# Kernel optimization log

Hardware: AMD Instinct MI355X
Metric: run time of the kernel (lower is better)

## Reference

```python
import jax, jax.numpy as jnp
import numpy as np

B, N, DIM, HEADS = 4, 1024, 1024, 16
DH = DIM // HEADS
SCALE = 1.0 / np.sqrt(DH)
EPS = 1e-6


def clinear(x, Wr, Wi, br, bi):
    # (a+bi)(Wr+Wi i): real = a Wr^T - b Wi^T, imag = a Wi^T + b Wr^T
    xr, xi = x.real, x.imag
    real = xr @ Wr.T - xi @ Wi.T + br
    imag = xr @ Wi.T + xi @ Wr.T + bi
    return jax.lax.complex(real, imag)


def cln(x, gamma, beta):
    # normalize magnitude over last dim, keep phase
    mag = jnp.abs(x)
    phase = jnp.angle(x)
    mean = jnp.mean(mag, axis=-1, keepdims=True)
    var = jnp.var(mag, axis=-1, keepdims=True)
    nm = (mag - mean) / jnp.sqrt(var + EPS)
    nm = nm * gamma + beta
    return jax.lax.complex(nm * jnp.cos(phase), nm * jnp.sin(phase))


def forward(xr, xi, Wq_r, Wq_i, bq_r, bq_i, Wk_r, Wk_i, bk_r, bk_i,
            Wv_r, Wv_i, bv_r, bv_i, Wo_r, Wo_i, bo_r, bo_i,
            gq, beq, gk, bek, gv, bev):
    x = jax.lax.complex(xr, xi)  # [B,N,D] complex64

    def heads(t):
        return t.reshape(B, N, HEADS, DH).transpose(0, 2, 1, 3)  # [B,H,N,dh]

    Q = heads(cln(clinear(x, Wq_r, Wq_i, bq_r, bq_i), gq, beq))
    K = heads(cln(clinear(x, Wk_r, Wk_i, bk_r, bk_i), gk, bek))
    V = heads(cln(clinear(x, Wv_r, Wv_i, bv_r, bv_i), gv, bev))

    Qf = jnp.fft.fft(Q, axis=2, norm='ortho')
    Kf = jnp.fft.fft(K, axis=2, norm='ortho')
    Vf = jnp.fft.fft(V, axis=2, norm='ortho')

    scores = jnp.einsum('bhnd,bhmd->bhnm', Qf, jnp.conj(Kf)) * SCALE
    attn = jax.nn.softmax(scores.real, axis=-1)  # real-valued softmax
    # attn is real; multiply into complex Vf componentwise
    out_f = jax.lax.complex(jnp.einsum('bhnm,bhmd->bhnd', attn, Vf.real),
                            jnp.einsum('bhnm,bhmd->bhnd', attn, Vf.imag))
    out = jnp.fft.ifft(out_f, axis=2, norm='ortho')
    out = out.transpose(0, 2, 1, 3).reshape(B, N, DIM)
    y = clinear(out, Wo_r, Wo_i, bo_r, bo_i)
    # return real||imag concatenated on last axis (float32 view of complex output)
    return jnp.concatenate([y.real, y.imag], axis=-1)


def setup_inputs() -> dict:
    key = jax.random.key(0)
    ks = jax.random.split(key, 16)
    wscale = np.sqrt(2.0 / (DIM + DIM)).astype(np.float32)
    d = {}
    d['xr'] = jax.random.normal(ks[0], (B, N, DIM), jnp.float32)
    d['xi'] = jax.random.normal(ks[1], (B, N, DIM), jnp.float32)
    i = 2
    for name in ('q', 'k', 'v', 'o'):
        d[f'W{name}_r'] = jax.random.normal(ks[i], (DIM, DIM), jnp.float32) * wscale; i += 1
        d[f'W{name}_i'] = jax.random.normal(ks[i], (DIM, DIM), jnp.float32) * wscale; i += 1
        d[f'b{name}_r'] = jnp.zeros((DIM,), jnp.float32)
        d[f'b{name}_i'] = jnp.zeros((DIM,), jnp.float32)
    for name in ('q', 'k', 'v'):
        d[f'g{name}'] = jnp.ones((DIM,), jnp.float32)
        d[f'be{name}'] = jnp.zeros((DIM,), jnp.float32)
    return d


def reference(xr, xi, Wq_r, Wq_i, bq_r, bq_i, Wk_r, Wk_i, bk_r, bk_i,
              Wv_r, Wv_i, bv_r, bv_i, Wo_r, Wo_i, bo_r, bo_i,
              gq, beq, gk, bek, gv, bev):
    return forward(xr, xi, Wq_r, Wq_i, bq_r, bq_i, Wk_r, Wk_i, bk_r, bk_i,
                   Wv_r, Wv_i, bv_r, bv_i, Wo_r, Wo_i, bo_r, bo_i,
                   gq, beq, gk, bek, gv, bev)
```

## Files before the change

kernel.cpp:

```cpp
#include <hip/hip_runtime.h>
#include <math.h>

#define BB 4
#define NN 1024
#define DIMM 1024
#define HHH 16
#define DHH 64
#define BN 4096
#define EPS_LN 1e-6f

typedef __bf16 bf16_t;
typedef __bf16 bf16x8 __attribute__((ext_vector_type(8)));
typedef __bf16 bf16x4 __attribute__((ext_vector_type(4)));
typedef float f32x4 __attribute__((ext_vector_type(4)));
typedef float f32x16 __attribute__((ext_vector_type(16)));
#define MFMA16(a, b, c) __builtin_amdgcn_mfma_f32_16x16x32_bf16(a, b, c, 0, 0, 0)
#define MFMA32(a, b, c) __builtin_amdgcn_mfma_f32_32x32x16_bf16(a, b, c, 0, 0, 0)
#define AS1 __attribute__((address_space(1)))
#define AS3 __attribute__((address_space(3)))

__device__ inline unsigned pk2(float a, float b) {
  union { bf16_t h[2]; unsigned u; } c;
  c.h[0] = (bf16_t)a; c.h[1] = (bf16_t)b;
  return c.u;
}
union U16 { uint4 u; bf16x8 v; };

__global__ __launch_bounds__(256) void pack_x(
    const float* __restrict__ xr, const float* __restrict__ xi,
    bf16_t* __restrict__ out)
{
  int t = blockIdx.x * 256 + threadIdx.x;
  size_t e = (size_t)t * 8;
  int row = (int)(e >> 11), col = (int)(e & 2047);
  const float* src = (col < 1024) ? (xr + (size_t)row * 1024 + col)
                                  : (xi + (size_t)row * 1024 + col - 1024);
  float4 a = *(const float4*)src;
  float4 b = *(const float4*)(src + 4);
  bf16x8 o;
  o[0] = (bf16_t)a.x; o[1] = (bf16_t)a.y; o[2] = (bf16_t)a.z; o[3] = (bf16_t)a.w;
  o[4] = (bf16_t)b.x; o[5] = (bf16_t)b.y; o[6] = (bf16_t)b.z; o[7] = (bf16_t)b.w;
  *(bf16x8*)(out + e) = o;
}

__global__ __launch_bounds__(256) void pack_w(
    const float* __restrict__ Wr, const float* __restrict__ Wi,
    const float* __restrict__ br, const float* __restrict__ bi,
    bf16_t* __restrict__ Wcat, float* __restrict__ bcat)
{
  int t = blockIdx.x * 256 + threadIdx.x;
  size_t e = (size_t)t * 8;
  int row = (int)(e >> 11), col = (int)(e & 2047);
  const float* src;
  float sgn = 1.f;
  if (row < 1024) {
    if (col < 1024) src = Wr + (size_t)row * 1024 + col;
    else          { src = Wi + (size_t)row * 1024 + col - 1024; sgn = -1.f; }
  } else {
    int r2 = row - 1024;
    if (col < 1024) src = Wi + (size_t)r2 * 1024 + col;
    else            src = Wr + (size_t)r2 * 1024 + col - 1024;
  }
  float4 a = *(const float4*)src;
  float4 b = *(const float4*)(src + 4);
  bf16x8 o;
  o[0] = (bf16_t)(sgn * a.x); o[1] = (bf16_t)(sgn * a.y);
  o[2] = (bf16_t)(sgn * a.z); o[3] = (bf16_t)(sgn * a.w);
  o[4] = (bf16_t)(sgn * b.x); o[5] = (bf16_t)(sgn * b.y);
  o[6] = (bf16_t)(sgn * b.z); o[7] = (bf16_t)(sgn * b.w);
  *(bf16x8*)(Wcat + e) = o;
  if (e < 2048) {
#pragma unroll
    for (int j = 0; j < 8; ++j) {
      int n = (int)e + j;
      bcat[n] = (n < 1024) ? br[n] : bi[n - 1024];
    }
  }
}

__global__ __launch_bounds__(256) void gemm_qkv(
    const bf16_t* __restrict__ A, const bf16_t* __restrict__ Bt,
    const float* __restrict__ bias, bf16_t* __restrict__ C6)
{
  __shared__ bf16_t sA[128 * 64];
  __shared__ bf16_t sB[128 * 64];
  const int tid = threadIdx.x;
  const int w = tid >> 6, l = tid & 63;
  const int lo4 = l & 15, hi = l >> 4;
  const int wr = w >> 1, wc = w & 1;
  const int row0 = blockIdx.y * 128, col0 = blockIdx.x * 128;

  const int srow = (l >> 3);
  const int scol = (l & 7) * 8;
  const bf16_t* gA[4];
  const bf16_t* gB[4];
#pragma unroll
  for (int i = 0; i < 4; ++i) {
    int r = (w * 4 + i) * 8 + srow;
    gA[i] = A  + (size_t)(row0 + r) * 2048 + scol;
    gB[i] = Bt + (size_t)(col0 + r) * 2048 + scol;
  }

  f32x4 acc[4][4] = {};
  for (int k0 = 0; k0 < 2048; k0 += 64) {
    __syncthreads();
#pragma unroll
    for (int i = 0; i < 4; ++i) {
      __builtin_amdgcn_global_load_lds((const AS1 void*)(gA[i] + k0),
                                       (AS3 void*)&sA[(w * 4 + i) * 512], 16, 0, 0);
      __builtin_amdgcn_global_load_lds((const AS1 void*)(gB[i] + k0),
                                       (AS3 void*)&sB[(w * 4 + i) * 512], 16, 0, 0);
    }
    __syncthreads();
#pragma unroll
    for (int kk = 0; kk < 2; ++kk) {
      bf16x8 am[4], bn[4];
#pragma unroll
      for (int i = 0; i < 4; ++i)
        am[i] = *(const bf16x8*)&sA[(wr * 64 + i * 16 + lo4) * 64 + kk * 32 + hi * 8];
#pragma unroll
      for (int j = 0; j < 4; ++j)
        bn[j] = *(const bf16x8*)&sB[(wc * 64 + j * 16 + lo4) * 64 + kk * 32 + hi * 8];
#pragma unroll
      for (int i = 0; i < 4; ++i)
#pragma unroll
        for (int j = 0; j < 4; ++j)
          acc[i][j] = MFMA16(am[i], bn[j], acc[i][j]);
    }
  }
  const int colg0 = col0 + wc * 64;
#pragma unroll
  for (int i = 0; i < 4; ++i) {
#pragma unroll
    for (int j = 0; j < 4; ++j) {
      float bv = bias[colg0 + j * 16 + lo4];
#pragma unroll
      for (int r = 0; r < 4; ++r) {
        int rowg = row0 + wr * 64 + i * 16 + hi * 4 + r;
        C6[(size_t)rowg * 6144 + colg0 + j * 16 + lo4] = (bf16_t)(acc[i][j][r] + bv);
      }
    }
  }
}

__global__ __launch_bounds__(256) void gemm_bf16(
    const bf16_t* __restrict__ A, const bf16_t* __restrict__ Bt,
    const float* __restrict__ bias,
    float* __restrict__ Cr, float* __restrict__ Ci, int ldc)
{
  __shared__ bf16_t sA[128 * 64];
  __shared__ bf16_t sB[128 * 64];
  const int tid = threadIdx.x;
  const int w = tid >> 6, l = tid & 63;
  const int lo4 = l & 15, hi = l >> 4;
  const int wr = w >> 1, wc = w & 1;
  const int row0 = blockIdx.y * 128, col0 = blockIdx.x * 128;

  const int srow = (l >> 3);
  const int scol = (l & 7) * 8;
  const bf16_t* gA[4];
  const bf16_t* gB[4];
#pragma unroll
  for (int i = 0; i < 4; ++i) {
    int r = (w * 4 + i) * 8 + srow;
    gA[i] = A  + (size_t)(row0 + r) * 2048 + scol;
    gB[i] = Bt + (size_t)(col0 + r) * 2048 + scol;
  }

  f32x4 acc[4][4] = {};
  for (int k0 = 0; k0 < 2048; k0 += 64) {
    __syncthreads();
#pragma unroll
    for (int i = 0; i < 4; ++i) {
      __builtin_amdgcn_global_load_lds((const AS1 void*)(gA[i] + k0),
                                       (AS3 void*)&sA[(w * 4 + i) * 512], 16, 0, 0);
      __builtin_amdgcn_global_load_lds((const AS1 void*)(gB[i] + k0),
                                       (AS3 void*)&sB[(w * 4 + i) * 512], 16, 0, 0);
    }
    __syncthreads();
#pragma unroll
    for (int kk = 0; kk < 2; ++kk) {
      bf16x8 am[4], bn[4];
#pragma unroll
      for (int i = 0; i < 4; ++i)
        am[i] = *(const bf16x8*)&sA[(wr * 64 + i * 16 + lo4) * 64 + kk * 32 + hi * 8];
#pragma unroll
      for (int j = 0; j < 4; ++j)
        bn[j] = *(const bf16x8*)&sB[(wc * 64 + j * 16 + lo4) * 64 + kk * 32 + hi * 8];
#pragma unroll
      for (int i = 0; i < 4; ++i)
#pragma unroll
        for (int j = 0; j < 4; ++j)
          acc[i][j] = MFMA16(am[i], bn[j], acc[i][j]);
    }
  }
  const int colg0 = col0 + wc * 64;
  float* Cp = (colg0 < 1024) ? Cr : Ci;
  const int cb = colg0 & 1023;
#pragma unroll
  for (int i = 0; i < 4; ++i) {
#pragma unroll
    for (int j = 0; j < 4; ++j) {
      float bv = bias[colg0 + j * 16 + lo4];
#pragma unroll
      for (int r = 0; r < 4; ++r) {
        int rowg = row0 + wr * 64 + i * 16 + hi * 4 + r;
        Cp[(size_t)rowg * ldc + cb + j * 16 + lo4] = acc[i][j][r] + bv;
      }
    }
  }
}

__global__ __launch_bounds__(256) void ln_stats3(
    const bf16_t* __restrict__ C6, float2* __restrict__ st)
{
  __shared__ float red[8];
  const int row = blockIdx.x;
  const int p = blockIdx.y;
  const int tid = threadIdx.x;
  const bf16_t* pr = C6 + (size_t)row * 6144 + p * 2048;
  const bf16_t* pi = pr + 1024;
  bf16x4 vr = *(const bf16x4*)(pr + tid * 4);
  bf16x4 vi = *(const bf16x4*)(pi + tid * 4);
  float s = 0.f, s2 = 0.f;
#pragma unroll
  for (int t = 0; t < 4; ++t) {
    float a = (float)vr[t], b = (float)vi[t];
    float mg = sqrtf(a * a + b * b);
    s += mg; s2 += mg * mg;
  }
#pragma unroll
  for (int o = 32; o; o >>= 1) { s += __shfl_down(s, o); s2 += __shfl_down(s2, o); }
  if ((tid & 63) == 0) { red[tid >> 6] = s; red[4 + (tid >> 6)] = s2; }
  __syncthreads();
  if (tid == 0) {
    float S = red[0] + red[1] + red[2] + red[3];
    float S2 = red[4] + red[5] + red[6] + red[7];
    float mean = S * (1.f / DIMM);
    float var = S2 * (1.f / DIMM) - mean * mean;
    st[(size_t)p * 4096 + row] = make_float2(mean, rsqrtf(var + EPS_LN));
  }
}

#define LIDX(d_, c_) (((d_) << 10) + ((c_) ^ (((c_) >> 5) & 31) ^ (((d_) & 7) << 2)))

__global__ __launch_bounds__(512) void fft_kernel(
    const bf16_t* __restrict__ inR, const bf16_t* __restrict__ inI,
    bf16_t* __restrict__ outR, bf16_t* __restrict__ outI,
    int in_sb, int in_sh, int in_sn, int in_sd,
    int out_sb, int out_sh, int out_sn,
    float sign, float oscale, int imode, int omode,
    const float2* __restrict__ stats,
    const float* __restrict__ gamma, const float* __restrict__ beta)
{
  __shared__ float lr[8 * 1024], li[8 * 1024];
  __shared__ float2 tw[1024];
  const int tid = threadIdx.x;
  const int dc = blockIdx.x & 7;
  const int bh = blockIdx.x >> 3;
  const int b = bh >> 4, h = bh & 15;
  const bf16_t* bR = inR + (size_t)b * in_sb + (size_t)h * in_sh;
  const bf16_t* bI = inI + (size_t)b * in_sb + (size_t)h * in_sh;
#pragma unroll
  for (int t = tid; t < 1024; t += 512) {
    float ang = sign * 3.14159265358979323846f * (float)t * (1.f / 512.f);
    float sn, cs;
    __sincosf(ang, &sn, &cs);
    tw[t] = make_float2(cs, sn);
  }
  if (imode == 0) {
    float gg[8], bb[8];
    if (stats) {
#pragma unroll
      for (int ds = 0; ds < 8; ++ds) {
        gg[ds] = gamma[h * DHH + dc * 8 + ds];
        bb[ds] = beta[h * DHH + dc * 8 + ds];
      }
    }
#pragma unroll
    for (int rep = 0; rep < 2; ++rep) {
      int n = tid + rep * 512;
      bf16x8 r8 = *(const bf16x8*)(bR + (size_t)n * in_sn + dc * 8);
      bf16x8 i8 = *(const bf16x8*)(bI + (size_t)n * in_sn + dc * 8);
      float ur[8], ui[8];
#pragma unroll
      for (int ds = 0; ds < 8; ++ds) { ur[ds] = (float)r8[ds]; ui[ds] = (float)i8[ds]; }
      if (stats) {
        float2 stv = stats[b * NN + n];
#pragma unroll
        for (int ds = 0; ds < 8; ++ds) {
          float a = ur[ds], c2 = ui[ds];
          float mag = sqrtf(a * a + c2 * c2);
          float nm = (mag - stv.x) * stv.y * gg[ds] + bb[ds];
          if (mag > 0.f) { float sc = nm / mag; ur[ds] = a * sc; ui[ds] = c2 * sc; }
          else           { ur[ds] = nm; ui[ds] = 0.f; }
        }
      }
#pragma unroll
      for (int ds = 0; ds < 8; ++ds) {
        int ax = LIDX(ds, n);
        lr[ax] = ur[ds];
        li[ax] = ui[ds];
      }
    }
  } else {
    const int ds = tid & 7, nb = tid >> 3;
    const bf16_t* pR = bR + (size_t)(dc * 8 + ds) * in_sd + nb * 16;
    const bf16_t* pI = bI + (size_t)(dc * 8 + ds) * in_sd + nb * 16;
    bf16x8 a0 = *(const bf16x8*)pR, a1 = *(const bf16x8*)(pR + 8);
    bf16x8 b0 = *(const bf16x8*)pI, b1 = *(const bf16x8*)(pI + 8);
#pragma unroll
    for (int k = 0; k < 8; ++k) {
      int c = nb * 16 + k;
      lr[LIDX(ds, c)] = (float)a0[k];       li[LIDX(ds, c)] = (float)b0[k];
      lr[LIDX(ds, c + 8)] = (float)a1[k];   li[LIDX(ds, c + 8)] = (float)b1[k];
    }
  }
  __syncthreads();
  const int dsub = tid & 7;
  const int jb = tid >> 3;
  int lq2 = 8;
  for (int st = 0; st < 5; ++st) {
    const int qtr = 1 << lq2;
    const int tmul = 1 << (2 * st);
    for (int jt = 0; jt < 4; ++jt) {
      int j = jb + jt * 64;
      int o = j & (qtr - 1);
      int i0 = ((j >> lq2) << (lq2 + 2)) + o;
      int a0 = LIDX(dsub, i0);
      int a1 = LIDX(dsub, i0 + qtr);
      int a2 = LIDX(dsub, i0 + 2 * qtr);
      int a3 = LIDX(dsub, i0 + 3 * qtr);
      float x0r = lr[a0], x0i = li[a0];
      float x1r = lr[a1], x1i = li[a1];
      float x2r = lr[a2], x2i = li[a2];
      float x3r = lr[a3], x3i = li[a3];
      float ar = x0r + x2r, ai2 = x0i + x2i;
      float br = x0r - x2r, bi  = x0i - x2i;
      float cr = x1r + x3r, ci  = x1i + x3i;
      float dr = x1r - x3r, di  = x1i - x3i;
      float2 t1 = tw[o * tmul];
      float2 t2 = tw[2 * o * tmul];
      float2 t3 = tw[3 * o * tmul];
      lr[a0] = ar + cr;  li[a0] = ai2 + ci;
      float u1r = br - sign * di, u1i = bi + sign * dr;
      lr[a1] = u1r * t1.x - u1i * t1.y;  li[a1] = u1r * t1.y + u1i * t1.x;
      float u2r = ar - cr, u2i = ai2 - ci;
      lr[a2] = u2r * t2.x - u2i * t2.y;  li[a2] = u2r * t2.y + u2i * t2.x;
      float u3r = br + sign * di, u3i = bi - sign * dr;
      lr[a3] = u3r * t3.x - u3i * t3.y;  li[a3] = u3r * t3.y + u3i * t3.x;
    }
    __syncthreads();
    lq2 -= 2;
  }
  bf16_t* oRb = outR + (size_t)b * out_sb + (size_t)h * out_sh;
  bf16_t* oIb = outI + (size_t)b * out_sb + (size_t)h * out_sh;
#pragma unroll
  for (int rep = 0; rep < 2; ++rep) {
    int n = tid + rep * 512;
    int rv2 = __brev((unsigned)n) >> 22;
    int p = ((rv2 & 0x155) << 1) | ((rv2 >> 1) & 0x155);
    float fr[8], fi[8];
#pragma unroll
    for (int ds = 0; ds < 8; ++ds) {
      fr[ds] = lr[LIDX(ds, p)] * oscale;
      fi[ds] = li[LIDX(ds, p)] * oscale;
    }
    if (omode == 1) {
      size_t tb = (size_t)(n >> 5) * 4096;
#pragma unroll
      for (int ds = 0; ds < 8; ++ds) {
        int dch = dc * 8 + ds;
        size_t ga = tb + (size_t)dch * 32 + ((n & 31) ^ (((dch >> 1) & 3) << 3));
        oRb[ga] = (bf16_t)fr[ds];
        oIb[ga] = (bf16_t)fi[ds];
      }
    } else {
      int cb = dc * 8;
      if (omode == 2) cb = (dc ^ (n & 7)) * 8;
      bf16x8 v0, w0;
#pragma unroll
      for (int k = 0; k < 8; ++k) {
        v0[k] = (bf16_t)fr[k];
        w0[k] = (bf16_t)fi[k];
      }
      size_t gb = (size_t)n * out_sn + cb;
      *(bf16x8*)(oRb + gb) = v0;
      *(bf16x8*)(oIb + gb) = w0;
    }
  }
}

__global__ __launch_bounds__(256, 2) void fattn(
    const bf16_t* __restrict__ Qf, const bf16_t* __restrict__ Kfs,
    const bf16_t* __restrict__ Vfs, bf16_t* __restrict__ OT)
{
  __shared__ bf16_t K3[3][4096];
  __shared__ bf16_t V3[3][4096];
  const int tid = threadIdx.x;
  const int w = tid >> 6, l = tid & 63;
  const int lq = l & 31;
  const int h = l >> 5;
  const int i = blockIdx.x;
  const int j = i >> 3;
  const int bh = (i & 7) * 8 + (j >> 3);
  const int q0 = (j & 7) * 128 + w * 32;

  bf16x8 bq[8];
  const bf16_t* qp = Qf + ((size_t)bh * NN + q0 + lq) * 128 + h * 8;
#pragma unroll
  for (int kk = 0; kk < 8; ++kk) bq[kk] = *(const bf16x8*)(qp + kk * 16);

  f32x16 o[4] = {};
  float m = -3e38f, ln = 0.f;

  const bf16_t* kg = Kfs + (size_t)bh * 131072 + w * 1024 + l * 8;
  const bf16_t* vg = Vfs + (size_t)bh * 131072 + w * 1024 + l * 8;
  const int kswz = (lq & 7) << 3;
  const int vswz = ((lq >> 1) & 3) << 3;

#pragma unroll
  for (int tt = 0; tt < 2; ++tt) {
    const bf16_t* kt = kg + (size_t)tt * 4096;
    const bf16_t* vt = vg + (size_t)tt * 4096;
#pragma unroll
    for (int ii = 0; ii < 2; ++ii) {
      __builtin_amdgcn_global_load_lds((const AS1 void*)(kt + ii * 512),
                                       (AS3 void*)&K3[tt][w * 1024 + ii * 512], 16, 0, 0);
      __builtin_amdgcn_global_load_lds((const AS1 void*)(vt + ii * 512),
                                       (AS3 void*)&V3[tt][w * 1024 + ii * 512], 16, 0, 0);
    }
  }
  asm volatile("s_waitcnt vmcnt(4)" ::: "memory");
  __builtin_amdgcn_s_barrier();
  __builtin_amdgcn_sched_barrier(0);

  int cur = 0;
  for (int t = 0; t < 32; ++t) {
    if (t < 30) {
      int nb = cur + 2; if (nb >= 3) nb -= 3;
      const bf16_t* kt = kg + (size_t)(t + 2) * 4096;
      const bf16_t* vt = vg + (size_t)(t + 2) * 4096;
#pragma unroll
      for (int ii = 0; ii < 2; ++ii) {
        __builtin_amdgcn_global_load_lds((const AS1 void*)(kt + ii * 512),
                                         (AS3 void*)&K3[nb][w * 1024 + ii * 512], 16, 0, 0);
        __builtin_amdgcn_global_load_lds((const AS1 void*)(vt + ii * 512),
                                         (AS3 void*)&V3[nb][w * 1024 + ii * 512], 16, 0, 0);
      }
    }

    f32x16 s = {};
#pragma unroll
    for (int kk = 0; kk < 8; ++kk) {
      bf16x8 ak = *(const bf16x8*)&K3[cur][lq * 128 + ((kk * 16 + h * 8) ^ kswz)];
      s = MFMA32(ak, bq[kk], s);
    }

    float pmax = s[0];
#pragma unroll
    for (int r = 1; r < 16; ++r) pmax = fmaxf(pmax, s[r]);
    pmax = fmaxf(pmax, __shfl_xor(pmax, 32));
    if (!__all(pmax - m <= 8.f)) {
      float mnew = fmaxf(m, pmax);
      float alpha = __expf(m - mnew);
      m = mnew;
      ln *= alpha;
#pragma unroll
      for (int db = 0; db < 4; ++db)
#pragma unroll
        for (int r = 0; r < 16; ++r) o[db][r] *= alpha;
    }
    float pf[16];
    float rs = 0.f;
#pragma unroll
    for (int r = 0; r < 16; ++r) { pf[r] = __expf(s[r] - m); rs += pf[r]; }
    rs += __shfl_xor(rs, 32);
    ln += rs;

    unsigned pw[8];
#pragma unroll
    for (int ii = 0; ii < 8; ++ii) pw[ii] = pk2(pf[2 * ii], pf[2 * ii + 1]);
    unsigned r0 = (unsigned)__shfl_xor((int)(h ? pw[0] : pw[2]), 32);
    unsigned r1 = (unsigned)__shfl_xor((int)(h ? pw[1] : pw[3]), 32);
    unsigned r2 = (unsigned)__shfl_xor((int)(h ? pw[4] : pw[6]), 32);
    unsigned r3 = (unsigned)__shfl_xor((int)(h ? pw[5] : pw[7]), 32);
    U16 bp0, bp1;
    bp0.u.x = h ? r0 : pw[0];  bp0.u.y = h ? r1 : pw[1];
    bp0.u.z = h ? pw[2] : r0;  bp0.u.w = h ? pw[3] : r1;
    bp1.u.x = h ? r2 : pw[4];  bp1.u.y = h ? r3 : pw[5];
    bp1.u.z = h ? pw[6] : r2;  bp1.u.w = h ? pw[7] : r3;

#pragma unroll
    for (int db = 0; db < 4; ++db) {
      int r = db * 32 + lq;
      bf16x8 av0 = *(const bf16x8*)&V3[cur][r * 32 + ((h * 8) ^ vswz)];
      bf16x8 av1 = *(const bf16x8*)&V3[cur][r * 32 + ((16 + h * 8) ^ vswz)];
      o[db] = MFMA32(av0, bp0.v, o[db]);
      o[db] = MFMA32(av1, bp1.v, o[db]);
    }

    if (t < 31) {
      if (t < 30) asm volatile("s_waitcnt vmcnt(4)" ::: "memory");
      else        asm volatile("s_waitcnt vmcnt(0)" ::: "memory");
      __builtin_amdgcn_s_barrier();
      __builtin_amdgcn_sched_barrier(0);
    }
    cur = (cur == 2) ? 0 : cur + 1;
  }

  float inv = 1.f / ln;
  const size_t otb = (size_t)bh * 128 * NN + q0 + lq;
#pragma unroll
  for (int db = 0; db < 4; ++db)
#pragma unroll
    for (int r = 0; r < 16; ++r) {
      int dl = (r & 3) + 8 * (r >> 2) + 4 * h;
      OT[otb + (size_t)(db * 32 + dl) * NN] = (bf16_t)(o[db][r] * inv);
    }
}

extern "C" void kernel_launch(void* const* d_in, const int* in_sizes, int n_in,
                              void* d_out, int out_size, void* d_ws, size_t ws_size,
                              hipStream_t stream) {
  const float* xr   = (const float*)d_in[0];
  const float* xi   = (const float*)d_in[1];
  const float* Wqr  = (const float*)d_in[2];
  const float* Wqi  = (const float*)d_in[3];
  const float* bqr  = (const float*)d_in[4];
  const float* bqi  = (const float*)d_in[5];
  const float* Wkr  = (const float*)d_in[6];
  const float* Wki  = (const float*)d_in[7];
  const float* bkr  = (const float*)d_in[8];
  const float* bki  = (const float*)d_in[9];
  const float* Wvr  = (const float*)d_in[10];
  const float* Wvi  = (const float*)d_in[11];
  const float* bvr  = (const float*)d_in[12];
  const float* bvi  = (const float*)d_in[13];
  const float* Wor  = (const float*)d_in[14];
  const float* Woi  = (const float*)d_in[15];
  const float* bor  = (const float*)d_in[16];
  const float* boi  = (const float*)d_in[17];
  const float* gq   = (const float*)d_in[18];
  const float* beq  = (const float*)d_in[19];
  const float* gk   = (const float*)d_in[20];
  const float* bek  = (const float*)d_in[21];
  const float* gv   = (const float*)d_in[22];
  const float* bev  = (const float*)d_in[23];

  char* wp = (char*)d_ws;
  bf16_t* Axaug = (bf16_t*)wp;  wp += (size_t)4096 * 2048 * 2;
  bf16_t* Wcat3 = (bf16_t*)wp;  wp += (size_t)6144 * 2048 * 2;
  float*  bcat3 = (float*)wp;   wp += (size_t)6144 * 4;
  float2* lnst3 = (float2*)wp;  wp += (size_t)3 * 4096 * 8;
  bf16_t* C6    = (bf16_t*)wp;  wp += (size_t)4096 * 6144 * 2;
  bf16_t* Qf    = (bf16_t*)wp;  wp += (size_t)64 * 1024 * 128 * 2;
  bf16_t* Kf    = (bf16_t*)wp;  wp += (size_t)64 * 1024 * 128 * 2;
  bf16_t* VfT   = (bf16_t*)wp;  wp += (size_t)64 * 1024 * 128 * 2;
  bf16_t* OT    = C6;
  bf16_t* Yaug  = Qf;

  const dim3 gQKV(48, 32);
  const dim3 gGemmO(16, 32);
  const int gPackX = (4096 * 2048 / 8) / 256;
  const int gPackW = (2048 * 2048 / 8) / 256;
  const dim3 gLn(4096, 3);
  const int gFft = 64 * 8;
  const int gAtt = 64 * 8;

  pack_x<<<gPackX, 256, 0, stream>>>(xr, xi, Axaug);
  pack_w<<<gPackW, 256, 0, stream>>>(Wqr, Wqi, bqr, bqi,
                                     Wcat3, bcat3);
  pack_w<<<gPackW, 256, 0, stream>>>(Wkr, Wki, bkr, bki,
                                     Wcat3 + (size_t)2048 * 2048, bcat3 + 2048);
  pack_w<<<gPackW, 256, 0, stream>>>(Wvr, Wvi, bvr, bvi,
                                     Wcat3 + (size_t)4096 * 2048, bcat3 + 4096);

  gemm_qkv<<<gQKV, 256, 0, stream>>>(Axaug, Wcat3, bcat3, C6);
  ln_stats3<<<gLn, 256, 0, stream>>>(C6, lnst3);

  fft_kernel<<<gFft, 512, 0, stream>>>(C6, C6 + 1024, Qf, Qf + 64,
      NN * 6144, DHH, 6144, 1,
      16 * NN * 128, NN * 128, 128,
      -1.0f, 0.03125f * 0.125f, 0, 0, lnst3, gq, beq);
  fft_kernel<<<gFft, 512, 0, stream>>>(C6 + 2048, C6 + 3072, Kf, Kf + 64,
      NN * 6144, DHH, 6144, 1,
      16 * NN * 128, NN * 128, 128,
      -1.0f, 0.03125f, 0, 2, lnst3 + 4096, gk, bek);
  fft_kernel<<<gFft, 512, 0, stream>>>(C6 + 4096, C6 + 5120, VfT, VfT + 2048,
      NN * 6144, DHH, 6144, 1,
      16 * 131072, 131072, 0,
      -1.0f, 0.03125f, 0, 1, lnst3 + 8192, gv, bev);

  fattn<<<gAtt, 256, 0, stream>>>(Qf, Kf, VfT, OT);

  fft_kernel<<<gFft, 512, 0, stream>>>(OT, OT + (size_t)64 * NN, Yaug, Yaug + 1024,
      16 * 128 * NN, 128 * NN, 1, NN,
      NN * 2048, 64, 2048,
      +1.0f, 0.03125f, 1, 0, nullptr, nullptr, nullptr);

  float* yout = (float*)d_out;
  pack_w<<<gPackW, 256, 0, stream>>>(Wor, Woi, bor, boi, Wcat3, bcat3);
  gemm_bf16<<<gGemmO, 256, 0, stream>>>(Yaug, Wcat3, bcat3, yout, yout + 1024, 2048);
}
```

Before: 410.1 us.

## Double-buffer LDS tiles in projection GEMMs with async prefetch two stages ahead

Both the QKV and output projection GEMMs now keep two LDS buffers for the A and B tiles. The global-to-LDS loads for tile t+2 are issued right after tile t is consumed, and an explicit vmcnt wait plus barrier sequences each buffer. This lets global memory latency overlap with MFMA work instead of stalling at every k-step. It doubles LDS use per block to 64KB, which may reduce occupancy.

```diff
diff --git a/kernel.cpp b/kernel.cpp
--- a/kernel.cpp
+++ b/kernel.cpp
@@ -82,8 +82,8 @@
     const bf16_t* __restrict__ A, const bf16_t* __restrict__ Bt,
     const float* __restrict__ bias, bf16_t* __restrict__ C6)
 {
-  __shared__ bf16_t sA[128 * 64];
-  __shared__ bf16_t sB[128 * 64];
+  __shared__ bf16_t sA[2][128 * 64];
+  __shared__ bf16_t sB[2][128 * 64];
   const int tid = threadIdx.x;
   const int w = tid >> 6, l = tid & 63;
   const int lo4 = l & 15, hi = l >> 4;
@@ -102,30 +102,54 @@
   }
 
   f32x4 acc[4][4] = {};
-  for (int k0 = 0; k0 < 2048; k0 += 64) {
-    __syncthreads();
-#pragma unroll
-    for (int i = 0; i < 4; ++i) {
-      __builtin_amdgcn_global_load_lds((const AS1 void*)(gA[i] + k0),
-                                       (AS3 void*)&sA[(w * 4 + i) * 512], 16, 0, 0);
-      __builtin_amdgcn_global_load_lds((const AS1 void*)(gB[i] + k0),
-                                       (AS3 void*)&sB[(w * 4 + i) * 512], 16, 0, 0);
-    }
-    __syncthreads();
+  const int nk = 2048 / 64;
+#pragma unroll
+  for (int i = 0; i < 4; ++i) {
+    __builtin_amdgcn_global_load_lds((const AS1 void*)(gA[i]),
+                                     (AS3 void*)&sA[0][(w * 4 + i) * 512], 16, 0, 0);
+    __builtin_amdgcn_global_load_lds((const AS1 void*)(gB[i]),
+                                     (AS3 void*)&sB[0][(w * 4 + i) * 512], 16, 0, 0);
+  }
+#pragma unroll
+  for (int i = 0; i < 4; ++i) {
+    __builtin_amdgcn_global_load_lds((const AS1 void*)(gA[i] + 64),
+                                     (AS3 void*)&sA[1][(w * 4 + i) * 512], 16, 0, 0);
+    __builtin_amdgcn_global_load_lds((const AS1 void*)(gB[i] + 64),
+                                     (AS3 void*)&sB[1][(w * 4 + i) * 512], 16, 0, 0);
+  }
+  for (int t = 0; t < nk; ++t) {
+    const int ct = t & 1;
+    if (t + 1 < nk) asm volatile("s_waitcnt vmcnt(8)" ::: "memory");
+    else            asm volatile("s_waitcnt vmcnt(0)" ::: "memory");
+    __builtin_amdgcn_sched_barrier(0);
+    __builtin_amdgcn_s_barrier();
+    __builtin_amdgcn_sched_barrier(0);
 #pragma unroll
     for (int kk = 0; kk < 2; ++kk) {
       bf16x8 am[4], bn[4];
 #pragma unroll
       for (int i = 0; i < 4; ++i)
-        am[i] = *(const bf16x8*)&sA[(wr * 64 + i * 16 + lo4) * 64 + kk * 32 + hi * 8];
+        am[i] = *(const bf16x8*)&sA[ct][(wr * 64 + i * 16 + lo4) * 64 + kk * 32 + hi * 8];
 #pragma unroll
       for (int j = 0; j < 4; ++j)
-        bn[j] = *(const bf16x8*)&sB[(wc * 64 + j * 16 + lo4) * 64 + kk * 32 + hi * 8];
+        bn[j] = *(const bf16x8*)&sB[ct][(wc * 64 + j * 16 + lo4) * 64 + kk * 32 + hi * 8];
 #pragma unroll
       for (int i = 0; i < 4; ++i)
 #pragma unroll
         for (int j = 0; j < 4; ++j)
           acc[i][j] = MFMA16(am[i], bn[j], acc[i][j]);
+    }
+    __builtin_amdgcn_s_barrier();
+    __builtin_amdgcn_sched_barrier(0);
+    if (t + 2 < nk) {
+      int k2 = (t + 2) * 64;
+#pragma unroll
+      for (int i = 0; i < 4; ++i) {
+        __builtin_amdgcn_global_load_lds((const AS1 void*)(gA[i] + k2),
+                                         (AS3 void*)&sA[ct][(w * 4 + i) * 512], 16, 0, 0);
+        __builtin_amdgcn_global_load_lds((const AS1 void*)(gB[i] + k2),
+                                         (AS3 void*)&sB[ct][(w * 4 + i) * 512], 16, 0, 0);
+      }
     }
   }
   const int colg0 = col0 + wc * 64;
@@ -148,8 +172,8 @@
     const float* __restrict__ bias,
     float* __restrict__ Cr, float* __restrict__ Ci, int ldc)
 {
-  __shared__ bf16_t sA[128 * 64];
-  __shared__ bf16_t sB[128 * 64];
+  __shared__ bf16_t sA[2][128 * 64];
+  __shared__ bf16_t sB[2][128 * 64];
   const int tid = threadIdx.x;
   const int w = tid >> 6, l = tid & 63;
   const int lo4 = l & 15, hi = l >> 4;
@@ -168,30 +192,54 @@
   }
 
   f32x4 acc[4][4] = {};
-  for (int k0 = 0; k0 < 2048; k0 += 64) {
-    __syncthreads();
-#pragma unroll
-    for (int i = 0; i < 4; ++i) {
-      __builtin_amdgcn_global_load_lds((const AS1 void*)(gA[i] + k0),
-                                       (AS3 void*)&sA[(w * 4 + i) * 512], 16, 0, 0);
-      __builtin_amdgcn_global_load_lds((const AS1 void*)(gB[i] + k0),
-                                       (AS3 void*)&sB[(w * 4 + i) * 512], 16, 0, 0);
-    }
-    __syncthreads();
+  const int nk = 2048 / 64;
+#pragma unroll
+  for (int i = 0; i < 4; ++i) {
+    __builtin_amdgcn_global_load_lds((const AS1 void*)(gA[i]),
+                                     (AS3 void*)&sA[0][(w * 4 + i) * 512], 16, 0, 0);
+    __builtin_amdgcn_global_load_lds((const AS1 void*)(gB[i]),
+                                     (AS3 void*)&sB[0][(w * 4 + i) * 512], 16, 0, 0);
+  }
+#pragma unroll
+  for (int i = 0; i < 4; ++i) {
+    __builtin_amdgcn_global_load_lds((const AS1 void*)(gA[i] + 64),
+                                     (AS3 void*)&sA[1][(w * 4 + i) * 512], 16, 0, 0);
+    __builtin_amdgcn_global_load_lds((const AS1 void*)(gB[i] + 64),
+                                     (AS3 void*)&sB[1][(w * 4 + i) * 512], 16, 0, 0);
+  }
+  for (int t = 0; t < nk; ++t) {
+    const int ct = t & 1;
+    if (t + 1 < nk) asm volatile("s_waitcnt vmcnt(8)" ::: "memory");
+    else            asm volatile("s_waitcnt vmcnt(0)" ::: "memory");
+    __builtin_amdgcn_sched_barrier(0);
+    __builtin_amdgcn_s_barrier();
+    __builtin_amdgcn_sched_barrier(0);
 #pragma unroll
     for (int kk = 0; kk < 2; ++kk) {
       bf16x8 am[4], bn[4];
 #pragma unroll
       for (int i = 0; i < 4; ++i)
-        am[i] = *(const bf16x8*)&sA[(wr * 64 + i * 16 + lo4) * 64 + kk * 32 + hi * 8];
+        am[i] = *(const bf16x8*)&sA[ct][(wr * 64 + i * 16 + lo4) * 64 + kk * 32 + hi * 8];
 #pragma unroll
       for (int j = 0; j < 4; ++j)
-        bn[j] = *(const bf16x8*)&sB[(wc * 64 + j * 16 + lo4) * 64 + kk * 32 + hi * 8];
+        bn[j] = *(const bf16x8*)&sB[ct][(wc * 64 + j * 16 + lo4) * 64 + kk * 32 + hi * 8];
 #pragma unroll
       for (int i = 0; i < 4; ++i)
 #pragma unroll
         for (int j = 0; j < 4; ++j)
           acc[i][j] = MFMA16(am[i], bn[j], acc[i][j]);
+    }
+    __builtin_amdgcn_s_barrier();
+    __builtin_amdgcn_sched_barrier(0);
+    if (t + 2 < nk) {
+      int k2 = (t + 2) * 64;
+#pragma unroll
+      for (int i = 0; i < 4; ++i) {
+        __builtin_amdgcn_global_load_lds((const AS1 void*)(gA[i] + k2),
+                                         (AS3 void*)&sA[ct][(w * 4 + i) * 512], 16, 0, 0);
+        __builtin_amdgcn_global_load_lds((const AS1 void*)(gB[i] + k2),
+                                         (AS3 void*)&sB[ct][(w * 4 + i) * 512], 16, 0, 0);
+      }
     }
   }
   const int colg0 = col0 + wc * 64;
```

Measured after the change: 402.6 us. About the same (-1.8%).

## Use Gauss three-multiplication trick for complex QKV projection GEMMs

Applied to the files above, without the earlier changes.

Replaces the 4-real-multiply complex QKV projection (one GEMM with K=2048) with Karatsuba/Gauss form: three K=1024 GEMMs per projection over packed inputs (xr+xi, xi, xr) and weights (Wr, Wr+Wi, Wi-Wr). The real and imaginary parts are rebuilt, with bias added, inside the LN-stats and FFT load stages. This cuts projection FLOPs by about a quarter, at the cost of larger intermediate buffers, extra reads in the consumers, and some added bf16 rounding error from summed operands. The output-weight packing is also moved before attention.

```diff
diff --git a/kernel.cpp b/kernel.cpp
--- a/kernel.cpp
+++ b/kernel.cpp
@@ -26,21 +26,58 @@
 }
 union U16 { uint4 u; bf16x8 v; };
 
-__global__ __launch_bounds__(256) void pack_x(
+__global__ __launch_bounds__(256) void pack_x3(
     const float* __restrict__ xr, const float* __restrict__ xi,
     bf16_t* __restrict__ out)
 {
   int t = blockIdx.x * 256 + threadIdx.x;
   size_t e = (size_t)t * 8;
-  int row = (int)(e >> 11), col = (int)(e & 2047);
-  const float* src = (col < 1024) ? (xr + (size_t)row * 1024 + col)
-                                  : (xi + (size_t)row * 1024 + col - 1024);
-  float4 a = *(const float4*)src;
-  float4 b = *(const float4*)(src + 4);
+  int row = (int)(e / 3072), col = (int)(e % 3072);
   bf16x8 o;
-  o[0] = (bf16_t)a.x; o[1] = (bf16_t)a.y; o[2] = (bf16_t)a.z; o[3] = (bf16_t)a.w;
-  o[4] = (bf16_t)b.x; o[5] = (bf16_t)b.y; o[6] = (bf16_t)b.z; o[7] = (bf16_t)b.w;
+  if (col < 1024) {
+    const float* pr = xr + (size_t)row * 1024 + col;
+    const float* pi = xi + (size_t)row * 1024 + col;
+    float4 a0 = *(const float4*)pr, a1 = *(const float4*)(pr + 4);
+    float4 b0 = *(const float4*)pi, b1 = *(const float4*)(pi + 4);
+    o[0] = (bf16_t)(a0.x + b0.x); o[1] = (bf16_t)(a0.y + b0.y);
+    o[2] = (bf16_t)(a0.z + b0.z); o[3] = (bf16_t)(a0.w + b0.w);
+    o[4] = (bf16_t)(a1.x + b1.x); o[5] = (bf16_t)(a1.y + b1.y);
+    o[6] = (bf16_t)(a1.z + b1.z); o[7] = (bf16_t)(a1.w + b1.w);
+  } else {
+    const float* src = (col < 2048) ? (xi + (size_t)row * 1024 + col - 1024)
+                                    : (xr + (size_t)row * 1024 + col - 2048);
+    float4 a0 = *(const float4*)src, a1 = *(const float4*)(src + 4);
+    o[0] = (bf16_t)a0.x; o[1] = (bf16_t)a0.y; o[2] = (bf16_t)a0.z; o[3] = (bf16_t)a0.w;
+    o[4] = (bf16_t)a1.x; o[5] = (bf16_t)a1.y; o[6] = (bf16_t)a1.z; o[7] = (bf16_t)a1.w;
+  }
   *(bf16x8*)(out + e) = o;
+}
+
+__global__ __launch_bounds__(256) void pack_w9(
+    const float* __restrict__ Wqr, const float* __restrict__ Wqi,
+    const float* __restrict__ Wkr, const float* __restrict__ Wki,
+    const float* __restrict__ Wvr, const float* __restrict__ Wvi,
+    bf16_t* __restrict__ W9)
+{
+  const int bz = blockIdx.y;
+  const int p = bz / 3, j = bz - p * 3;
+  const float* Wr = (p == 0) ? Wqr : (p == 1) ? Wkr : Wvr;
+  const float* Wi = (p == 0) ? Wqi : (p == 1) ? Wki : Wvi;
+  int t = blockIdx.x * 256 + threadIdx.x;
+  size_t e = (size_t)t * 8;
+  const float* pr = Wr + e;
+  const float* pi = Wi + e;
+  float4 a0 = *(const float4*)pr, a1 = *(const float4*)(pr + 4);
+  float4 b0 = *(const float4*)pi, b1 = *(const float4*)(pi + 4);
+  float v0[8] = {a0.x, a0.y, a0.z, a0.w, a1.x, a1.y, a1.z, a1.w};
+  float v1[8] = {b0.x, b0.y, b0.z, b0.w, b1.x, b1.y, b1.z, b1.w};
+  bf16x8 o;
+#pragma unroll
+  for (int k = 0; k < 8; ++k) {
+    float v = (j == 0) ? v0[k] : (j == 1) ? (v0[k] + v1[k]) : (v1[k] - v0[k]);
+    o[k] = (bf16_t)v;
+  }
+  *(bf16x8*)(W9 + (size_t)bz * 1048576 + e) = o;
 }
 
 __global__ __launch_bounds__(256) void pack_w(
@@ -78,9 +115,9 @@
   }
 }
 
-__global__ __launch_bounds__(256) void gemm_qkv(
-    const bf16_t* __restrict__ A, const bf16_t* __restrict__ Bt,
-    const float* __restrict__ bias, bf16_t* __restrict__ C6)
+__global__ __launch_bounds__(256) void gemm_k3(
+    const bf16_t* __restrict__ Ax3, const bf16_t* __restrict__ W9,
+    bf16_t* __restrict__ C9)
 {
   __shared__ bf16_t sA[128 * 64];
   __shared__ bf16_t sB[128 * 64];
@@ -89,6 +126,11 @@
   const int lo4 = l & 15, hi = l >> 4;
   const int wr = w >> 1, wc = w & 1;
   const int row0 = blockIdx.y * 128, col0 = blockIdx.x * 128;
+  const int bz = blockIdx.z;
+  const int p = bz / 3, j = bz - p * 3;
+
+  const bf16_t* Abase = Ax3 + (size_t)j * 1024;
+  const bf16_t* Bbase = W9 + (size_t)bz * 1048576;
 
   const int srow = (l >> 3);
   const int scol = (l & 7) * 8;
@@ -97,12 +139,12 @@
 #pragma unroll
   for (int i = 0; i < 4; ++i) {
     int r = (w * 4 + i) * 8 + srow;
-    gA[i] = A  + (size_t)(row0 + r) * 2048 + scol;
-    gB[i] = Bt + (size_t)(col0 + r) * 2048 + scol;
+    gA[i] = Abase + (size_t)(row0 + r) * 3072 + scol;
+    gB[i] = Bbase + (size_t)(col0 + r) * 1024 + scol;
   }
 
   f32x4 acc[4][4] = {};
-  for (int k0 = 0; k0 < 2048; k0 += 64) {
+  for (int k0 = 0; k0 < 1024; k0 += 64) {
     __syncthreads();
 #pragma unroll
     for (int i = 0; i < 4; ++i) {
@@ -119,25 +161,25 @@
       for (int i = 0; i < 4; ++i)
         am[i] = *(const bf16x8*)&sA[(wr * 64 + i * 16 + lo4) * 64 + kk * 32 + hi * 8];
 #pragma unroll
-      for (int j = 0; j < 4; ++j)
-        bn[j] = *(const bf16x8*)&sB[(wc * 64 + j * 16 + lo4) * 64 + kk * 32 + hi * 8];
+      for (int jf = 0; jf < 4; ++jf)
+        bn[jf] = *(const bf16x8*)&sB[(wc * 64 + jf * 16 + lo4) * 64 + kk * 32 + hi * 8];
 #pragma unroll
       for (int i = 0; i < 4; ++i)
 #pragma unroll
-        for (int j = 0; j < 4; ++j)
-          acc[i][j] = MFMA16(am[i], bn[j], acc[i][j]);
-    }
-  }
+        for (int jf = 0; jf < 4; ++jf)
+          acc[i][jf] = MFMA16(am[i], bn[jf], acc[i][jf]);
+    }
+  }
+  bf16_t* Cb = C9 + (size_t)p * 3072 + (size_t)j * 1024;
   const int colg0 = col0 + wc * 64;
 #pragma unroll
   for (int i = 0; i < 4; ++i) {
 #pragma unroll
-    for (int j = 0; j < 4; ++j) {
-      float bv = bias[colg0 + j * 16 + lo4];
+    for (int jf = 0; jf < 4; ++jf) {
 #pragma unroll
       for (int r = 0; r < 4; ++r) {
         int rowg = row0 + wr * 64 + i * 16 + hi * 4 + r;
-        C6[(size_t)rowg * 6144 + colg0 + j * 16 + lo4] = (bf16_t)(acc[i][j][r] + bv);
+        Cb[(size_t)rowg * 9216 + colg0 + jf * 16 + lo4] = (bf16_t)acc[i][jf][r];
       }
     }
   }
@@ -211,22 +253,29 @@
   }
 }
 
-__global__ __launch_bounds__(256) void ln_stats3(
-    const bf16_t* __restrict__ C6, float2* __restrict__ st)
+__global__ __launch_bounds__(256) void ln_stats3m(
+    const bf16_t* __restrict__ C9, float2* __restrict__ st,
+    const float* __restrict__ bqr, const float* __restrict__ bqi,
+    const float* __restrict__ bkr, const float* __restrict__ bki,
+    const float* __restrict__ bvr, const float* __restrict__ bvi)
 {
   __shared__ float red[8];
   const int row = blockIdx.x;
   const int p = blockIdx.y;
   const int tid = threadIdx.x;
-  const bf16_t* pr = C6 + (size_t)row * 6144 + p * 2048;
-  const bf16_t* pi = pr + 1024;
-  bf16x4 vr = *(const bf16x4*)(pr + tid * 4);
-  bf16x4 vi = *(const bf16x4*)(pi + tid * 4);
+  const float* br = (p == 0) ? bqr : (p == 1) ? bkr : bvr;
+  const float* bi = (p == 0) ? bqi : (p == 1) ? bki : bvi;
+  const bf16_t* base = C9 + (size_t)row * 9216 + (size_t)p * 3072 + tid * 4;
+  bf16x4 m1 = *(const bf16x4*)base;
+  bf16x4 m2 = *(const bf16x4*)(base + 1024);
+  bf16x4 m3 = *(const bf16x4*)(base + 2048);
   float s = 0.f, s2 = 0.f;
 #pragma unroll
   for (int t = 0; t < 4; ++t) {
-    float a = (float)vr[t], b = (float)vi[t];
-    float mg = sqrtf(a * a + b * b);
+    int c = tid * 4 + t;
+    float re = (float)m1[t] - (float)m2[t] + br[c];
+    float im = (float)m1[t] + (float)m3[t] + bi[c];
+    float mg = sqrtf(re * re + im * im);
     s += mg; s2 += mg * mg;
   }
 #pragma unroll
@@ -247,11 +296,12 @@
 __global__ __launch_bounds__(512) void fft_kernel(
     const bf16_t* __restrict__ inR, const bf16_t* __restrict__ inI,
     bf16_t* __restrict__ outR, bf16_t* __restrict__ outI,
-    int in_sb, int in_sh, int in_sn, int in_sd,
+    long in_sb, int in_sh, int in_sn, int in_sd,
     int out_sb, int out_sh, int out_sn,
     float sign, float oscale, int imode, int omode,
     const float2* __restrict__ stats,
-    const float* __restrict__ gamma, const float* __restrict__ beta)
+    const float* __restrict__ gamma, const float* __restrict__ beta,
+    const float* __restrict__ biasr, const float* __restrict__ biasi)
 {
   __shared__ float lr[8 * 1024], li[8 * 1024];
   __shared__ float2 tw[1024];
@@ -268,39 +318,33 @@
     __sincosf(ang, &sn, &cs);
     tw[t] = make_float2(cs, sn);
   }
-  if (imode == 0) {
-    float gg[8], bb[8];
-    if (stats) {
-#pragma unroll
-      for (int ds = 0; ds < 8; ++ds) {
-        gg[ds] = gamma[h * DHH + dc * 8 + ds];
-        bb[ds] = beta[h * DHH + dc * 8 + ds];
-      }
+  if (imode == 2) {
+    float gg[8], bb[8], brv[8], biv[8];
+#pragma unroll
+    for (int ds = 0; ds < 8; ++ds) {
+      int dim = h * DHH + dc * 8 + ds;
+      gg[ds] = gamma[dim];  bb[ds] = beta[dim];
+      brv[ds] = biasr[dim]; biv[ds] = biasi[dim];
     }
 #pragma unroll
     for (int rep = 0; rep < 2; ++rep) {
       int n = tid + rep * 512;
-      bf16x8 r8 = *(const bf16x8*)(bR + (size_t)n * in_sn + dc * 8);
-      bf16x8 i8 = *(const bf16x8*)(bI + (size_t)n * in_sn + dc * 8);
-      float ur[8], ui[8];
-#pragma unroll
-      for (int ds = 0; ds < 8; ++ds) { ur[ds] = (float)r8[ds]; ui[ds] = (float)i8[ds]; }
-      if (stats) {
-        float2 stv = stats[b * NN + n];
-#pragma unroll
-        for (int ds = 0; ds < 8; ++ds) {
-          float a = ur[ds], c2 = ui[ds];
-          float mag = sqrtf(a * a + c2 * c2);
-          float nm = (mag - stv.x) * stv.y * gg[ds] + bb[ds];
-          if (mag > 0.f) { float sc = nm / mag; ur[ds] = a * sc; ui[ds] = c2 * sc; }
-          else           { ur[ds] = nm; ui[ds] = 0.f; }
-        }
-      }
+      const bf16_t* pb = bR + (size_t)n * in_sn + dc * 8;
+      bf16x8 m1 = *(const bf16x8*)pb;
+      bf16x8 m2 = *(const bf16x8*)(pb + 1024);
+      bf16x8 m3 = *(const bf16x8*)(pb + 2048);
+      float2 stv = stats[b * NN + n];
 #pragma unroll
       for (int ds = 0; ds < 8; ++ds) {
+        float re = (float)m1[ds] - (float)m2[ds] + brv[ds];
+        float im = (float)m1[ds] + (float)m3[ds] + biv[ds];
+        float mag = sqrtf(re * re + im * im);
+        float nm = (mag - stv.x) * stv.y * gg[ds] + bb[ds];
+        if (mag > 0.f) { float sc = nm / mag; re *= sc; im *= sc; }
+        else           { re = nm; im = 0.f; }
         int ax = LIDX(ds, n);
-        lr[ax] = ur[ds];
-        li[ax] = ui[ds];
+        lr[ax] = re;
+        li[ax] = im;
       }
     }
   } else {
@@ -549,57 +593,57 @@
   const float* bev  = (const float*)d_in[23];
 
   char* wp = (char*)d_ws;
-  bf16_t* Axaug = (bf16_t*)wp;  wp += (size_t)4096 * 2048 * 2;
-  bf16_t* Wcat3 = (bf16_t*)wp;  wp += (size_t)6144 * 2048 * 2;
-  float*  bcat3 = (float*)wp;   wp += (size_t)6144 * 4;
+  bf16_t* Ax3   = (bf16_t*)wp;  wp += (size_t)4096 * 3072 * 2;
+  bf16_t* W9    = (bf16_t*)wp;  wp += (size_t)9 * 1048576 * 2;
+  float*  bcatO = (float*)wp;   wp += (size_t)2048 * 4;
   float2* lnst3 = (float2*)wp;  wp += (size_t)3 * 4096 * 8;
-  bf16_t* C6    = (bf16_t*)wp;  wp += (size_t)4096 * 6144 * 2;
+  bf16_t* C9    = (bf16_t*)wp;  wp += (size_t)4096 * 9216 * 2;
   bf16_t* Qf    = (bf16_t*)wp;  wp += (size_t)64 * 1024 * 128 * 2;
   bf16_t* Kf    = (bf16_t*)wp;  wp += (size_t)64 * 1024 * 128 * 2;
   bf16_t* VfT   = (bf16_t*)wp;  wp += (size_t)64 * 1024 * 128 * 2;
-  bf16_t* OT    = C6;
+  bf16_t* OT    = C9;
+  bf16_t* WcatO = C9 + (size_t)16 * 1048576;
   bf16_t* Yaug  = Qf;
 
-  const dim3 gQKV(48, 32);
+  const dim3 gK3(8, 32, 9);
   const dim3 gGemmO(16, 32);
-  const int gPackX = (4096 * 2048 / 8) / 256;
-  const int gPackW = (2048 * 2048 / 8) / 256;
+  const int gPackX = (4096 * 3072 / 8) / 256;
+  const dim3 gPackW9(512, 9);
+  const int gPackWO = (2048 * 2048 / 8) / 256;
   const dim3 gLn(4096, 3);
   const int gFft = 64 * 8;
   const int gAtt = 64 * 8;
-
-  pack_x<<<gPackX, 256, 0, stream>>>(xr, xi, Axaug);
-  pack_w<<<gPackW, 256, 0, stream>>>(Wqr, Wqi, bqr, bqi,
-                                     Wcat3, bcat3);
-  pack_w<<<gPackW, 256, 0, stream>>>(Wkr, Wki, bkr, bki,
-                                     Wcat3 + (size_t)2048 * 2048, bcat3 + 2048);
-  pack_w<<<gPackW, 256, 0, stream>>>(Wvr, Wvi, bvr, bvi,
-                                     Wcat3 + (size_t)4096 * 2048, bcat3 + 4096);
-
-  gemm_qkv<<<gQKV, 256, 0, stream>>>(Axaug, Wcat3, bcat3, C6);
-  ln_stats3<<<gLn, 256, 0, stream>>>(C6, lnst3);
-
-  fft_kernel<<<gFft, 512, 0, stream>>>(C6, C6 + 1024, Qf, Qf + 64,
-      NN * 6144, DHH, 6144, 1,
+  const long c9sb = (long)NN * 9216;
+
+  pack_x3<<<gPackX, 256, 0, stream>>>(xr, xi, Ax3);
+  pack_w9<<<gPackW9, 256, 0, stream>>>(Wqr, Wqi, Wkr, Wki, Wvr, Wvi, W9);
+
+  gemm_k3<<<gK3, 256, 0, stream>>>(Ax3, W9, C9);
+  ln_stats3m<<<gLn, 256, 0, stream>>>(C9, lnst3, bqr, bqi, bkr, bki, bvr, bvi);
+
+  fft_kernel<<<gFft, 512, 0, stream>>>(C9, C9, Qf, Qf + 64,
+      c9sb, DHH, 9216, 1,
       16 * NN * 128, NN * 128, 128,
-      -1.0f, 0.03125f * 0.125f, 0, 0, lnst3, gq, beq);
-  fft_kernel<<<gFft, 512, 0, stream>>>(C6 + 2048, C6 + 3072, Kf, Kf + 64,
-      NN * 6144, DHH, 6144, 1,
+      -1.0f, 0.03125f * 0.125f, 2, 0, lnst3, gq, beq, bqr, bqi);
+  fft_kernel<<<gFft, 512, 0, stream>>>(C9 + 3072, C9, Kf, Kf + 64,
+      c9sb, DHH, 9216, 1,
       16 * NN * 128, NN * 128, 128,
-      -1.0f, 0.03125f, 0, 2, lnst3 + 4096, gk, bek);
-  fft_kernel<<<gFft, 512, 0, stream>>>(C6 + 4096, C6 + 5120, VfT, VfT + 2048,
-      NN * 6144, DHH, 6144, 1,
+      -1.0f, 0.03125f, 2, 2, lnst3 + 4096, gk, bek, bkr, bki);
+  fft_kernel<<<gFft, 512, 0, stream>>>(C9 + 6144, C9, VfT, VfT + 2048,
+      c9sb, DHH, 9216, 1,
       16 * 131072, 131072, 0,
-      -1.0f, 0.03125f, 0, 1, lnst3 + 8192, gv, bev);
+      -1.0f, 0.03125f, 2, 1, lnst3 + 8192, gv, bev, bvr, bvi);
+
+  pack_w<<<gPackWO, 256, 0, stream>>>(Wor, Woi, bor, boi, WcatO, bcatO);
 
   fattn<<<gAtt, 256, 0, stream>>>(Qf, Kf, VfT, OT);
 
   fft_kernel<<<gFft, 512, 0, stream>>>(OT, OT + (size_t)64 * NN, Yaug, Yaug + 1024,
-      16 * 128 * NN, 128 * NN, 1, NN,
+      (long)16 * 128 * NN, 128 * NN, 1, NN,
       NN * 2048, 64, 2048,
-      +1.0f, 0.03125f, 1, 0, nullptr, nullptr, nullptr);
+      +1.0f, 0.03125f, 1, 0, nullptr, nullptr, nullptr, nullptr, nullptr);
 
   float* yout = (float*)d_out;
-  pack_w<<<gPackW, 256, 0, stream>>>(Wor, Woi, bor, boi, Wcat3, bcat3);
-  gemm_bf16<<<gGemmO, 256, 0, stream>>>(Yaug, Wcat3, bcat3, yout, yout + 1024, 2048);
-}
+  gemm_bf16<<<gGemmO, 256, 0, stream>>>(Yaug, WcatO, bcatO,
+                                        yout, yout + 1024, 2048);
+}
```

Result: slower. 423.0 us (+3.1%).
